# Kernel optimization log

Hardware: AMD Instinct MI355X
Metric: run time of the kernel (lower is better)

## Reference

```python
import jax, jax.numpy as jnp
import numpy as np

B, C, H, W = 4, 256, 64, 64
DQK = C // 4


def setup_inputs() -> dict:
    key = jax.random.key(0)
    ks = jax.random.split(key, 5)
    s = 0.05
    x = jax.random.normal(ks[0], (B, C, H, W), dtype=jnp.float32)
    Wq = jax.random.normal(ks[1], (DQK, C), dtype=jnp.float32) * s
    Wk = jax.random.normal(ks[2], (DQK, C), dtype=jnp.float32) * s
    Wv = jax.random.normal(ks[3], (C, C), dtype=jnp.float32) * s
    bq = jnp.zeros((DQK,), jnp.float32)
    bk = jnp.zeros((DQK,), jnp.float32)
    bv = jnp.zeros((C,), jnp.float32)
    gamma = jnp.zeros((1,), jnp.float32)
    return {"x": x, "Wq": Wq, "bq": bq, "Wk": Wk, "bk": bk,
            "Wv": Wv, "bv": bv, "gamma": gamma}


def reference(x, Wq, bq, Wk, bk, Wv, bv, gamma):
    b, c, h, w = x.shape
    n = h * w
    xf = x.reshape(b, c, n)                      # [B, C, N]
    # 1x1 convs == per-pixel linear projections
    q = jnp.einsum('dc,bcn->bnd', Wq, xf) + bq   # [B, N, Dqk]
    k = jnp.einsum('dc,bcn->bdn', Wk, xf) + bk[None, :, None]  # [B, Dqk, N]
    v = jnp.einsum('ec,bcn->ben', Wv, xf) + bv[None, :, None]  # [B, C, N]
    energy = jnp.einsum('bnd,bdm->bnm', q, k)    # [B, N, N]
    attn = jax.nn.softmax(energy, axis=-1)       # softmax over keys
    # out[b,c,i] = sum_j v[b,c,j] * attn[b,i,j]
    out = jnp.einsum('bcj,bij->bci', v, attn)    # [B, C, N]
    out = out.reshape(b, c, h, w)
    return gamma * out + x
```

## Files before the change

kernel.cpp:

```cpp
#include <hip/hip_runtime.h>

#define B_ 4
#define C_ 256
#define N_ 4096
#define D_ 64

typedef __bf16 bf16x8 __attribute__((ext_vector_type(8)));
typedef float floatx4 __attribute__((ext_vector_type(4)));
typedef unsigned short ushort8v __attribute__((ext_vector_type(8)));
typedef unsigned short ushort4v __attribute__((ext_vector_type(4)));
typedef unsigned short ushort2v __attribute__((ext_vector_type(2)));

static __device__ __forceinline__ unsigned short f2bf(float f) {
    unsigned int u = __builtin_bit_cast(unsigned int, f);
    u += 0x7fffu + ((u >> 16) & 1u);
    return (unsigned short)(u >> 16);
}
static __device__ __forceinline__ float bf2f(unsigned short h) {
    unsigned int u = ((unsigned int)h) << 16;
    return __builtin_bit_cast(float, u);
}
static __device__ __forceinline__ unsigned int cvt_pk_bf16(float lo, float hi) {
    unsigned int d;
    asm("v_cvt_pk_bf16_f32 %0, %1, %2" : "=v"(d) : "v"(lo), "v"(hi));
    return d;
}

#define GLOAD16(gp, lp)                                                      \
    __builtin_amdgcn_global_load_lds(                                        \
        (const __attribute__((address_space(1))) void*)(gp),                 \
        (__attribute__((address_space(3))) void*)(lp), 16, 0, 0)

__global__ __launch_bounds__(256) void convert_w(
    const float* __restrict__ Wq, const float* __restrict__ Wk,
    const float* __restrict__ Wv, unsigned short* __restrict__ WbfA)
{
    int tid = blockIdx.x * 256 + threadIdx.x;
    int p0  = tid * 4;
    int j0   = p0 & 7;
    int lane = (p0 >> 3) & 63;
    int sidx = p0 >> 9;
    int ft = sidx >> 3, ks = sidx & 7;
    int m  = lane & 15, g = lane >> 4;
    int f  = 16*ft + m;
    int c  = 32*ks + 8*g + j0;
    const float* src = (f < 64)  ? (Wq + (size_t)f * C_)
                     : (f < 128) ? (Wk + (size_t)(f - 64) * C_)
                                 : (Wv + (size_t)(f - 128) * C_);
    float4 v = *(const float4*)(src + c);
    uint2 u;
    u.x = cvt_pk_bf16(v.x, v.y);
    u.y = cvt_pk_bf16(v.z, v.w);
    *(uint2*)(WbfA + p0) = u;
}

__global__ __launch_bounds__(256, 3) void proj_kernel(
    const float* __restrict__ x, const unsigned short* __restrict__ WbfA,
    const float* __restrict__ bq, const float* __restrict__ bk,
    const float* __restrict__ bv,
    unsigned short* __restrict__ Qg, unsigned short* __restrict__ Kg,
    unsigned short* __restrict__ Vg)
{
    __shared__ __align__(16) unsigned short smem[64 * 264];
    unsigned short* xs = smem;
    unsigned short* Lt = smem;

    const int n0 = blockIdx.x * 64;
    const int f0 = blockIdx.y * 128;
    const int b  = blockIdx.z;
    const int t  = threadIdx.x;
    const int w  = t >> 6;
    const int lane = t & 63;
    const int g  = lane >> 4;
    const int m  = lane & 15;

#pragma unroll
    for (int k = 0; k < 8; ++k) {
        int e  = t + 256 * k;
        int cp = e >> 4;
        int c  = 2 * cp;
        int n4 = (e & 15) * 4;
        float4 v0 = *(const float4*)(x + ((size_t)b*C_ + c    )*N_ + n0 + n4);
        float4 v1 = *(const float4*)(x + ((size_t)b*C_ + c + 1)*N_ + n0 + n4);
        float a0[4] = {v0.x, v0.y, v0.z, v0.w};
        float a1[4] = {v1.x, v1.y, v1.z, v1.w};
#pragma unroll
        for (int j = 0; j < 4; ++j) {
            int n = n4 + j;
            unsigned int u = cvt_pk_bf16(a0[j], a1[j]);
            *(unsigned int*)&xs[n*264 + (((c >> 3) ^ (n & 7)) << 3) + (c & 7)] = u;
        }
    }

    float bias_[2][4];
#pragma unroll
    for (int mt = 0; mt < 2; ++mt)
#pragma unroll
        for (int r = 0; r < 4; ++r) {
            int fg = f0 + 32*w + 16*mt + 4*g + r;
            bias_[mt][r] = (fg < 64) ? bq[fg]
                         : (fg < 128) ? bk[fg - 64] : bv[fg - 128];
        }

    const unsigned short* Wa0 = WbfA + (size_t)(((f0 >> 4) + 2*w    )*8)*512
                              + lane*8;
    const unsigned short* Wa1 = WbfA + (size_t)(((f0 >> 4) + 2*w + 1)*8)*512
                              + lane*8;

    floatx4 acc[2][4];
#pragma unroll
    for (int mt = 0; mt < 2; ++mt)
#pragma unroll
        for (int nt = 0; nt < 4; ++nt) acc[mt][nt] = (floatx4){0.f,0.f,0.f,0.f};

    __syncthreads();

#pragma unroll
    for (int ks = 0; ks < 8; ++ks) {
        bf16x8 af[2];
        af[0] = *(const bf16x8*)(Wa0 + ks*512);
        af[1] = *(const bf16x8*)(Wa1 + ks*512);
#pragma unroll
        for (int nt = 0; nt < 4; ++nt) {
            int n = 16*nt + m;
            bf16x8 bfr = *(const bf16x8*)
                &xs[n*264 + (((4*ks + g) ^ (n & 7)) << 3)];
#pragma unroll
            for (int mt = 0; mt < 2; ++mt)
                acc[mt][nt] = __builtin_amdgcn_mfma_f32_16x16x32_bf16(
                                  af[mt], bfr, acc[mt][nt], 0, 0, 0);
        }
    }

    __syncthreads();

#pragma unroll
    for (int mt = 0; mt < 2; ++mt)
#pragma unroll
        for (int nt = 0; nt < 4; ++nt)
#pragma unroll
            for (int r = 0; r < 4; ++r)
                Lt[(32*w + 16*mt + 4*g + r)*72 + 16*nt + m] =
                    f2bf(acc[mt][nt][r] + bias_[mt][r]);
    __syncthreads();

    if (f0 == 0) {
#pragma unroll
        for (int k = 0; k < 4; ++k) {
            int e   = t + 256 * k;
            int fq0 = (e >> 6) * 8;
            int nl  = e & 63;
            ushort8v u;
#pragma unroll
            for (int j = 0; j < 8; ++j) u[j] = Lt[(fq0 + j)*72 + nl];
            unsigned short* dst = (fq0 < 64)
                ? (Qg + ((size_t)b*N_ + n0 + nl)*D_ + fq0)
                : (Kg + ((size_t)b*N_ + n0 + nl)*D_ + (fq0 - 64));
            *(ushort8v*)dst = u;
        }
    } else {
        const int cb = f0 - 128;
#pragma unroll
        for (int k = 0; k < 4; ++k) {
            int e  = t + 256 * k;
            int fr = e >> 3;
            int n8 = (e & 7) * 8;
            ushort8v u = *(const ushort8v*)&Lt[fr*72 + n8];
            *(ushort8v*)(Vg + ((size_t)b*C_ + cb + fr)*N_ + n0 + n8) = u;
        }
    }
}

__global__ __launch_bounds__(512, 2) void flash_kernel(
    const unsigned short* __restrict__ Qg, const unsigned short* __restrict__ Kg,
    const unsigned short* __restrict__ Vg,
    unsigned short* __restrict__ Opart, float* __restrict__ ML)
{
    __shared__ __align__(16) unsigned short Vlds[32 * 512];
    __shared__ __align__(16) unsigned short Klds[2][8 * 512];
    __shared__ __align__(16) unsigned short PA[16 * 64 * 8];
    __shared__ float AL[128];

    const int g8   = blockIdx.x;
    const int tile = blockIdx.y;
    const int half = g8 & 1;
    const int b    = g8 >> 1;
    const int n0   = tile * 128;
    const int t    = threadIdx.x;
    const int w    = t >> 6;
    const int lane = t & 63;
    const int g    = lane >> 4;
    const int m    = lane & 15;
    const int wq   = w >> 2;
    const int cq   = w & 3;

    const unsigned short* Qb = Qg + ((size_t)b*N_ + n0)*D_;
    const unsigned short* Kb = Kg + (size_t)b*N_*D_;
    const unsigned short* Vb = Vg + (size_t)b*C_*N_;

    const int cstart = half * 32;
    const int cend   = cstart + 32;

    bf16x8 qf[2];
#pragma unroll
    for (int ks = 0; ks < 2; ++ks)
        qf[ks] = *(const bf16x8*)(Qb + (size_t)(16*w + m)*D_ + 32*ks + 8*g);

    floatx4 accO[4][4];
#pragma unroll
    for (int rt = 0; rt < 4; ++rt)
#pragma unroll
        for (int ct = 0; ct < 4; ++ct)
            accO[rt][ct] = (floatx4){0.f, 0.f, 0.f, 0.f};

    float mrow = -1e30f, lrow = 0.f;

    {
        const unsigned short* gp =
            Kb + (size_t)(cstart*64 + 16*(w >> 1) + m)*D_ + 32*(w & 1) + 8*g;
        GLOAD16(gp, &Klds[0][w * 512]);
    }
    __syncthreads();

    for (int t64 = cstart; t64 < cend; ++t64) {
        const int j0 = t64 * 64;
        const int kb = (t64 - cstart) & 1;

#pragma unroll
        for (int u = 0; u < 4; ++u) {
            int sidx = 4*w + u;
            int ks   = sidx >> 4;
            int cb   = sidx & 15;
            const unsigned short* gp =
                Vb + (size_t)(16*cb + m)*N_ + j0 + 32*ks + 8*g;
            GLOAD16(gp, &Vlds[sidx * 512]);
        }
        if (t64 + 1 < cend) {
            const unsigned short* gp =
                Kb + (size_t)((t64+1)*64 + 16*(w >> 1) + m)*D_
                   + 32*(w & 1) + 8*g;
            GLOAD16(gp, &Klds[kb ^ 1][w * 512]);
        }

        floatx4 accST[4];
#pragma unroll
        for (int jt = 0; jt < 4; ++jt) accST[jt] = (floatx4){0.f,0.f,0.f,0.f};
#pragma unroll
        for (int ks = 0; ks < 2; ++ks)
#pragma unroll
            for (int jt = 0; jt < 4; ++jt) {
                bf16x8 kfr = *(const bf16x8*)
                    &Klds[kb][(jt*2 + ks)*512 + lane*8];
                accST[jt] = __builtin_amdgcn_mfma_f32_16x16x32_bf16(
                                kfr, qf[ks], accST[jt], 0, 0, 0);
            }

        float mx = -1e30f;
#pragma unroll
        for (int jt = 0; jt < 4; ++jt)
#pragma unroll
            for (int r = 0; r < 4; ++r) mx = fmaxf(mx, accST[jt][r]);
        mx = fmaxf(mx, __shfl_xor(mx, 16));
        mx = fmaxf(mx, __shfl_xor(mx, 32));
        float mnew  = fmaxf(mrow, mx);
        float alpha = __expf(mrow - mnew);
        mrow = mnew;
        float p[4][4];
        float rs = 0.f;
#pragma unroll
        for (int jt = 0; jt < 4; ++jt)
#pragma unroll
            for (int r = 0; r < 4; ++r) {
                float e = __expf(accST[jt][r] - mnew);
                p[jt][r] = e;
                rs += e;
            }
        rs += __shfl_xor(rs, 16);
        rs += __shfl_xor(rs, 32);
        lrow = lrow * alpha + rs;

        if (g == 0) AL[16*w + m] = alpha;

#pragma unroll
        for (int jt = 0; jt < 4; ++jt) {
            uint2 pu;
            pu.x = cvt_pk_bf16(p[jt][0], p[jt][1]);
            pu.y = cvt_pk_bf16(p[jt][2], p[jt][3]);
            int frag = (w*2 + (jt >> 1))*64 + 16*(2*(jt & 1) + (g >> 1)) + m;
            *(uint2*)&PA[frag*8 + 4*(g & 1)] = pu;
        }

        __syncthreads();

#pragma unroll
        for (int rt = 0; rt < 4; ++rt) {
            floatx4 a4 = *(const floatx4*)&AL[64*wq + 16*rt + 4*g];
#pragma unroll
            for (int ct = 0; ct < 4; ++ct)
                accO[rt][ct] *= a4;
        }
#pragma unroll
        for (int ks = 0; ks < 2; ++ks) {
            bf16x8 pf[4];
#pragma unroll
            for (int rt = 0; rt < 4; ++rt)
                pf[rt] = *(const bf16x8*)
                    &PA[((8*wq + rt*2 + ks)*64 + lane)*8];
#pragma unroll
            for (int ct = 0; ct < 4; ++ct) {
                int sidx = ks*16 + 4*cq + ct;
                bf16x8 vfrag = *(const bf16x8*)&Vlds[sidx*512 + lane*8];
#pragma unroll
                for (int rt = 0; rt < 4; ++rt)
                    accO[rt][ct] = __builtin_amdgcn_mfma_f32_16x16x32_bf16(
                                       pf[rt], vfrag, accO[rt][ct], 0, 0, 0);
            }
        }

        __syncthreads();
    }

    const size_t tbase = ((size_t)(half*B_ + b)*32 + tile);
    unsigned short* Ob = Opart + tbase * (C_ * 128);
    float* ml = ML + tbase * 256;

    if (g == 0) {
        ml[16*w + m]       = mrow;
        ml[128 + 16*w + m] = lrow;
    }

#pragma unroll
    for (int rt = 0; rt < 4; ++rt)
#pragma unroll
        for (int ct = 0; ct < 4; ++ct) {
            int c  = 64*cq + 16*ct + m;
            int q0 = 64*wq + 16*rt + 4*g;
            uint2 pu;
            pu.x = cvt_pk_bf16(accO[rt][ct][0], accO[rt][ct][1]);
            pu.y = cvt_pk_bf16(accO[rt][ct][2], accO[rt][ct][3]);
            *(uint2*)(Ob + (size_t)c*128 + q0) = pu;
        }
}

__global__ __launch_bounds__(256) void combine_kernel(
    const unsigned short* __restrict__ Opart, const float* __restrict__ ML,
    const float* __restrict__ x, const float* __restrict__ gamma,
    float* __restrict__ out)
{
    __shared__ float sc0[128], sc1[128];
    const int tile   = blockIdx.x;
    const int cslice = blockIdx.y;
    const int b      = blockIdx.z;
    const int n0     = tile * 128;
    const int t      = threadIdx.x;

    if (t < 128) {
        const float* ml0 = ML + ((size_t)(0*B_ + b)*32 + tile)*256;
        const float* ml1 = ML + ((size_t)(1*B_ + b)*32 + tile)*256;
        float m0 = ml0[t], l0 = ml0[128 + t];
        float m1 = ml1[t], l1 = ml1[128 + t];
        float M  = fmaxf(m0, m1);
        float f0 = __expf(m0 - M), f1 = __expf(m1 - M);
        float L  = f0*l0 + f1*l1;
        float gm = gamma[0];
        sc0[t] = gm * f0 / L;
        sc1[t] = gm * f1 / L;
    }
    __syncthreads();

    const int nq = t & 31;
    const int cl = t >> 5;
    const float* xb = x   + (size_t)b*C_*N_;
    float*       ob = out + (size_t)b*C_*N_;
    const unsigned short* O0 = Opart + ((size_t)(0*B_ + b)*32 + tile)*(C_*128);
    const unsigned short* O1 = Opart + ((size_t)(1*B_ + b)*32 + tile)*(C_*128);

    float s0[4], s1[4];
#pragma unroll
    for (int k = 0; k < 4; ++k) { s0[k] = sc0[4*nq + k]; s1[k] = sc1[4*nq + k]; }

#pragma unroll
    for (int i = 0; i < 4; ++i) {
        int c = 32*cslice + 8*i + cl;
        float4 x4 = *(const float4*)(xb + (size_t)c*N_ + n0 + 4*nq);
        ushort4v a4 = *(const ushort4v*)(O0 + (size_t)c*128 + 4*nq);
        ushort4v b4 = *(const ushort4v*)(O1 + (size_t)c*128 + 4*nq);
        float4 y;
        y.x = s0[0]*bf2f(a4[0]) + s1[0]*bf2f(b4[0]) + x4.x;
        y.y = s0[1]*bf2f(a4[1]) + s1[1]*bf2f(b4[1]) + x4.y;
        y.z = s0[2]*bf2f(a4[2]) + s1[2]*bf2f(b4[2]) + x4.z;
        y.w = s0[3]*bf2f(a4[3]) + s1[3]*bf2f(b4[3]) + x4.w;
        *(float4*)(ob + (size_t)c*N_ + n0 + 4*nq) = y;
    }
}

extern "C" void kernel_launch(void* const* d_in, const int* in_sizes, int n_in,
                              void* d_out, int out_size, void* d_ws, size_t ws_size,
                              hipStream_t stream) {
    const float* x     = (const float*)d_in[0];
    const float* Wq    = (const float*)d_in[1];
    const float* bq    = (const float*)d_in[2];
    const float* Wk    = (const float*)d_in[3];
    const float* bk    = (const float*)d_in[4];
    const float* Wv    = (const float*)d_in[5];
    const float* bv    = (const float*)d_in[6];
    const float* gamma = (const float*)d_in[7];
    float* out = (float*)d_out;

    unsigned short* Qg = (unsigned short*)d_ws;
    unsigned short* Kg = Qg + (size_t)B_*N_*D_;
    unsigned short* Vg = Kg + (size_t)B_*N_*D_;
    unsigned short* Op = Vg + (size_t)B_*C_*N_;
    float* ML = (float*)(Op + (size_t)2*B_*32*C_*128);
    unsigned short* WbfA = (unsigned short*)(ML + (size_t)2*B_*32*256);

    convert_w<<<dim3(96), 256, 0, stream>>>(Wq, Wk, Wv, WbfA);
    proj_kernel<<<dim3(64, 3, 4), 256, 0, stream>>>(x, WbfA, bq, bk, bv,
                                                    Qg, Kg, Vg);
    flash_kernel<<<dim3(8, 32), 512, 0, stream>>>(Qg, Kg, Vg, Op, ML);
    combine_kernel<<<dim3(32, 8, 4), 256, 0, stream>>>(Op, ML, x, gamma, out);
}
```

Measured before the change: 179.8 us.

## Fuse weight conversion into projection and combine into flash via last-block atomic

The separate weight-conversion kernel is removed, and each projection block now loads fp32 weight rows directly and converts them to bf16 fragments in registers. The combine kernel is also removed. The second of the two flash blocks that finish a tile merges the two partial outputs and writes the result, after an atomic counter plus threadfences. This cuts two kernel launches and their gaps, at the cost of redundant weight conversion in every projection block, higher register pressure, and a serialized combine tail done by half the flash blocks with fewer threads per tile.

Measured after the change: 260.1 us. 1.45x slower.

```diff
diff --git a/kernel.cpp b/kernel.cpp
--- a/kernel.cpp
+++ b/kernel.cpp
@@ -31,35 +31,14 @@
         (const __attribute__((address_space(1))) void*)(gp),                 \
         (__attribute__((address_space(3))) void*)(lp), 16, 0, 0)
 
-__global__ __launch_bounds__(256) void convert_w(
+__global__ __launch_bounds__(256, 3) void proj_kernel(
+    const float* __restrict__ x,
     const float* __restrict__ Wq, const float* __restrict__ Wk,
-    const float* __restrict__ Wv, unsigned short* __restrict__ WbfA)
-{
-    int tid = blockIdx.x * 256 + threadIdx.x;
-    int p0  = tid * 4;
-    int j0   = p0 & 7;
-    int lane = (p0 >> 3) & 63;
-    int sidx = p0 >> 9;
-    int ft = sidx >> 3, ks = sidx & 7;
-    int m  = lane & 15, g = lane >> 4;
-    int f  = 16*ft + m;
-    int c  = 32*ks + 8*g + j0;
-    const float* src = (f < 64)  ? (Wq + (size_t)f * C_)
-                     : (f < 128) ? (Wk + (size_t)(f - 64) * C_)
-                                 : (Wv + (size_t)(f - 128) * C_);
-    float4 v = *(const float4*)(src + c);
-    uint2 u;
-    u.x = cvt_pk_bf16(v.x, v.y);
-    u.y = cvt_pk_bf16(v.z, v.w);
-    *(uint2*)(WbfA + p0) = u;
-}
-
-__global__ __launch_bounds__(256, 3) void proj_kernel(
-    const float* __restrict__ x, const unsigned short* __restrict__ WbfA,
+    const float* __restrict__ Wv,
     const float* __restrict__ bq, const float* __restrict__ bk,
     const float* __restrict__ bv,
     unsigned short* __restrict__ Qg, unsigned short* __restrict__ Kg,
-    unsigned short* __restrict__ Vg)
+    unsigned short* __restrict__ Vg, int* __restrict__ flags)
 {
     __shared__ __align__(16) unsigned short smem[64 * 264];
     unsigned short* xs = smem;
@@ -73,6 +52,9 @@
     const int lane = t & 63;
     const int g  = lane >> 4;
     const int m  = lane & 15;
+
+    if (blockIdx.x == 0 && blockIdx.y == 0 && t < 32)
+        flags[b * 32 + t] = 0;
 
 #pragma unroll
     for (int k = 0; k < 8; ++k) {
@@ -102,10 +84,29 @@
                          : (fg < 128) ? bk[fg - 64] : bv[fg - 128];
         }
 
-    const unsigned short* Wa0 = WbfA + (size_t)(((f0 >> 4) + 2*w    )*8)*512
-                              + lane*8;
-    const unsigned short* Wa1 = WbfA + (size_t)(((f0 >> 4) + 2*w + 1)*8)*512
-                              + lane*8;
+    const int fr0 = f0 + 32*w + m;
+    const int fr1 = fr0 + 16;
+    const float* wr0 = (fr0 < 64) ? Wq + (size_t)fr0*C_
+                     : (fr0 < 128)? Wk + (size_t)(fr0 - 64)*C_
+                                  : Wv + (size_t)(fr0 - 128)*C_;
+    const float* wr1 = (fr1 < 64) ? Wq + (size_t)fr1*C_
+                     : (fr1 < 128)? Wk + (size_t)(fr1 - 64)*C_
+                                  : Wv + (size_t)(fr1 - 128)*C_;
+    bf16x8 afr[2][8];
+#pragma unroll
+    for (int ks = 0; ks < 8; ++ks) {
+        float4 l0 = *(const float4*)(wr0 + 32*ks + 8*g);
+        float4 h0 = *(const float4*)(wr0 + 32*ks + 8*g + 4);
+        float4 l1 = *(const float4*)(wr1 + 32*ks + 8*g);
+        float4 h1 = *(const float4*)(wr1 + 32*ks + 8*g + 4);
+        uint4 u0, u1;
+        u0.x = cvt_pk_bf16(l0.x, l0.y); u0.y = cvt_pk_bf16(l0.z, l0.w);
+        u0.z = cvt_pk_bf16(h0.x, h0.y); u0.w = cvt_pk_bf16(h0.z, h0.w);
+        u1.x = cvt_pk_bf16(l1.x, l1.y); u1.y = cvt_pk_bf16(l1.z, l1.w);
+        u1.z = cvt_pk_bf16(h1.x, h1.y); u1.w = cvt_pk_bf16(h1.z, h1.w);
+        afr[0][ks] = __builtin_bit_cast(bf16x8, u0);
+        afr[1][ks] = __builtin_bit_cast(bf16x8, u1);
+    }
 
     floatx4 acc[2][4];
 #pragma unroll
@@ -117,9 +118,6 @@
 
 #pragma unroll
     for (int ks = 0; ks < 8; ++ks) {
-        bf16x8 af[2];
-        af[0] = *(const bf16x8*)(Wa0 + ks*512);
-        af[1] = *(const bf16x8*)(Wa1 + ks*512);
 #pragma unroll
         for (int nt = 0; nt < 4; ++nt) {
             int n = 16*nt + m;
@@ -128,7 +126,7 @@
 #pragma unroll
             for (int mt = 0; mt < 2; ++mt)
                 acc[mt][nt] = __builtin_amdgcn_mfma_f32_16x16x32_bf16(
-                                  af[mt], bfr, acc[mt][nt], 0, 0, 0);
+                                  afr[mt][ks], bfr, acc[mt][nt], 0, 0, 0);
         }
     }
 
@@ -174,7 +172,9 @@
 __global__ __launch_bounds__(512, 2) void flash_kernel(
     const unsigned short* __restrict__ Qg, const unsigned short* __restrict__ Kg,
     const unsigned short* __restrict__ Vg,
-    unsigned short* __restrict__ Opart, float* __restrict__ ML)
+    unsigned short* __restrict__ Opart, float* __restrict__ ML,
+    int* __restrict__ flags, const float* __restrict__ x,
+    const float* __restrict__ gamma, float* __restrict__ out)
 {
     __shared__ __align__(16) unsigned short Vlds[32 * 512];
     __shared__ __align__(16) unsigned short Klds[2][8 * 512];
@@ -340,20 +340,18 @@
             pu.y = cvt_pk_bf16(accO[rt][ct][2], accO[rt][ct][3]);
             *(uint2*)(Ob + (size_t)c*128 + q0) = pu;
         }
-}
-
-__global__ __launch_bounds__(256) void combine_kernel(
-    const unsigned short* __restrict__ Opart, const float* __restrict__ ML,
-    const float* __restrict__ x, const float* __restrict__ gamma,
-    float* __restrict__ out)
-{
-    __shared__ float sc0[128], sc1[128];
-    const int tile   = blockIdx.x;
-    const int cslice = blockIdx.y;
-    const int b      = blockIdx.z;
-    const int n0     = tile * 128;
-    const int t      = threadIdx.x;
-
+
+    __threadfence();
+    __syncthreads();
+    __shared__ int amLast;
+    if (t == 0) amLast = (atomicAdd(&flags[b*32 + tile], 1) == 1);
+    __syncthreads();
+    if (!amLast) return;
+    __threadfence();
+
+    float* scbuf = (float*)&Klds[0][0];
+    float* sc0_ = scbuf;
+    float* sc1_ = scbuf + 128;
     if (t < 128) {
         const float* ml0 = ML + ((size_t)(0*B_ + b)*32 + tile)*256;
         const float* ml1 = ML + ((size_t)(1*B_ + b)*32 + tile)*256;
@@ -363,8 +361,8 @@
         float f0 = __expf(m0 - M), f1 = __expf(m1 - M);
         float L  = f0*l0 + f1*l1;
         float gm = gamma[0];
-        sc0[t] = gm * f0 / L;
-        sc1[t] = gm * f1 / L;
+        sc0_[t] = gm * f0 / L;
+        sc1_[t] = gm * f1 / L;
     }
     __syncthreads();
 
@@ -377,11 +375,11 @@
 
     float s0[4], s1[4];
 #pragma unroll
-    for (int k = 0; k < 4; ++k) { s0[k] = sc0[4*nq + k]; s1[k] = sc1[4*nq + k]; }
-
-#pragma unroll
-    for (int i = 0; i < 4; ++i) {
-        int c = 32*cslice + 8*i + cl;
+    for (int k = 0; k < 4; ++k) { s0[k] = sc0_[4*nq + k]; s1[k] = sc1_[4*nq + k]; }
+
+#pragma unroll 4
+    for (int i = 0; i < 16; ++i) {
+        int c = 16*i + cl;
         float4 x4 = *(const float4*)(xb + (size_t)c*N_ + n0 + 4*nq);
         ushort4v a4 = *(const ushort4v*)(O0 + (size_t)c*128 + 4*nq);
         ushort4v b4 = *(const ushort4v*)(O1 + (size_t)c*128 + 4*nq);
@@ -412,11 +410,11 @@
     unsigned short* Vg = Kg + (size_t)B_*N_*D_;
     unsigned short* Op = Vg + (size_t)B_*C_*N_;
     float* ML = (float*)(Op + (size_t)2*B_*32*C_*128);
-    unsigned short* WbfA = (unsigned short*)(ML + (size_t)2*B_*32*256);
-
-    convert_w<<<dim3(96), 256, 0, stream>>>(Wq, Wk, Wv, WbfA);
-    proj_kernel<<<dim3(64, 3, 4), 256, 0, stream>>>(x, WbfA, bq, bk, bv,
-                                                    Qg, Kg, Vg);
-    flash_kernel<<<dim3(8, 32), 512, 0, stream>>>(Qg, Kg, Vg, Op, ML);
-    combine_kernel<<<dim3(32, 8, 4), 256, 0, stream>>>(Op, ML, x, gamma, out);
-}
+    int* flags = (int*)(ML + (size_t)2*B_*32*256);
+
+    proj_kernel<<<dim3(64, 3, 4), 256, 0, stream>>>(x, Wq, Wk, Wv,
+                                                    bq, bk, bv,
+                                                    Qg, Kg, Vg, flags);
+    flash_kernel<<<dim3(8, 32), 512, 0, stream>>>(Qg, Kg, Vg, Op, ML,
+                                                  flags, x, gamma, out);
+}
```
